# Kernel tuning notes

Measured on AMD Instinct MI355X. Metric: run time of the kernel, lower is better.

The kernel has to match this reference:

```python
import jax, jax.numpy as jnp
import numpy as np

N_NODES = 50000
D = 128
N_POS = 400000
N_NEG = 200000  # N_NODES * neg_k(4)
E = N_POS + N_NEG


def setup_inputs() -> dict:
    key = jax.random.key(0)
    k_x, k_w1, k_w2, k_p = jax.random.split(key, 4)
    x = jax.random.normal(k_x, (N_NODES, D), dtype=jnp.float32)
    # torch nn.Linear params: y = x @ W.T + b
    W1 = jax.random.normal(k_w1, (D, 2 * D), dtype=jnp.float32) * (1.0 / np.sqrt(2 * D))
    b1 = jnp.zeros((D,), dtype=jnp.float32)
    W2 = jax.random.normal(k_w2, (1, D), dtype=jnp.float32) * (1.0 / np.sqrt(D))
    b2 = jnp.zeros((1,), dtype=jnp.float32)
    pairs = jax.random.randint(k_p, (2, E), 0, N_NODES, dtype=jnp.int64)
    labels = jnp.concatenate([jnp.ones((N_POS,), jnp.float32), jnp.zeros((N_NEG,), jnp.float32)])
    return {"x": x, "W1": W1, "b1": b1, "W2": W2, "b2": b2, "labels": labels, "pairs": pairs}


def reference(x, W1, b1, W2, b2, labels, pairs):
    us, vs = pairs[0], pairs[1]
    # edge gather + concat: [E, 2D]
    feats = jnp.concatenate([x[us], x[vs]], axis=-1)
    h = jax.nn.relu(feats @ W1.T + b1)            # [E, D]
    z = (h @ W2.T + b2).ravel()                   # [E] logits
    # binary_cross_entropy_with_logits, mean reduction (numerically stable)
    loss = -jnp.mean(labels * jax.nn.log_sigmoid(z) + (1.0 - labels) * jax.nn.log_sigmoid(-z))
    return loss
```

## Files before the change

### kernel.cpp

```cpp
#include <hip/hip_runtime.h>
#include <hip/hip_fp16.h>

#define D 128
#define TWO_D 256

typedef _Float16 half2v __attribute__((ext_vector_type(2)));
typedef _Float16 half8v __attribute__((ext_vector_type(8)));
typedef float floatx4 __attribute__((ext_vector_type(4)));

__device__ inline unsigned int pkrtz(float a, float b) {
    return __builtin_bit_cast(unsigned int, __builtin_amdgcn_cvt_pkrtz(a, b));
}

__global__ __launch_bounds__(256) void gemm_nodes(
        const float* __restrict__ x, const float* __restrict__ W1,
        const float* __restrict__ b1,
        unsigned char* __restrict__ AB, float* __restrict__ out0, int nNodes) {
    const int tid  = threadIdx.x;
    const int wave = tid >> 6, lane = tid & 63;
    const int quad = lane >> 4, l16 = lane & 15;
    const int nb0  = blockIdx.x * 64;

    if (blockIdx.x == 0 && tid == 0) *out0 = 0.f;

    half8v Bf[4][4];
    float bias[4];
#pragma unroll
    for (int t = 0; t < 4; ++t) {
        const int o = wave * 64 + t * 16 + l16;
        bias[t] = (o < D) ? b1[o] : 0.f;
        const float* wrow = (o < D) ? (W1 + (size_t)o * TWO_D)
                                    : (W1 + (size_t)(o - D) * TWO_D + D);
#pragma unroll
        for (int ks = 0; ks < 4; ++ks) {
            const float* wp = wrow + ks * 32 + quad * 8;
            floatx4 w0 = *(const floatx4*)wp;
            floatx4 w1v = *(const floatx4*)(wp + 4);
            uint4 pk;
            pk.x = pkrtz(w0[0], w0[1]);  pk.y = pkrtz(w0[2], w0[3]);
            pk.z = pkrtz(w1v[0], w1v[1]); pk.w = pkrtz(w1v[2], w1v[3]);
            Bf[t][ks] = __builtin_bit_cast(half8v, pk);
        }
    }

    __shared__ __align__(16) unsigned short xs[16][136];
    __shared__ __align__(16) float ct[16][260];

    const int srow = tid >> 4;
    const int sc8  = tid & 15;

    floatx4 v0, v1;
    {
        const int node = nb0 + srow;
        const int nc = node < nNodes ? node : nNodes - 1;
        const float* xp = x + (size_t)nc * D + sc8 * 8;
        v0 = *(const floatx4*)xp;
        v1 = *(const floatx4*)(xp + 4);
    }

    for (int sub = 0; sub < 4; ++sub) {
        __syncthreads();
        uint4 pk;
        pk.x = pkrtz(v0[0], v0[1]);  pk.y = pkrtz(v0[2], v0[3]);
        pk.z = pkrtz(v1[0], v1[1]);  pk.w = pkrtz(v1[2], v1[3]);
        *(uint4*)&xs[srow][sc8 * 8] = pk;
        __syncthreads();

        if (sub < 3) {
            const int node = nb0 + (sub + 1) * 16 + srow;
            const int nc = node < nNodes ? node : nNodes - 1;
            const float* xp = x + (size_t)nc * D + sc8 * 8;
            v0 = *(const floatx4*)xp;
            v1 = *(const floatx4*)(xp + 4);
        }

        half8v Af[4];
#pragma unroll
        for (int ks = 0; ks < 4; ++ks)
            Af[ks] = *(const half8v*)&xs[l16][ks * 32 + quad * 8];

        floatx4 acc[4];
#pragma unroll
        for (int t = 0; t < 4; ++t) acc[t] = (floatx4){0.f, 0.f, 0.f, 0.f};
#pragma unroll
        for (int ks = 0; ks < 4; ++ks)
#pragma unroll
            for (int t = 0; t < 4; ++t)
                acc[t] = __builtin_amdgcn_mfma_f32_16x16x32_f16(Af[ks], Bf[t][ks], acc[t], 0, 0, 0);

#pragma unroll
        for (int t = 0; t < 4; ++t) {
            const int o = wave * 64 + t * 16 + l16;
#pragma unroll
            for (int r = 0; r < 4; ++r)
                ct[quad * 4 + r][o] = acc[t][r] + bias[t];
        }
        __syncthreads();

        const int nrow = nb0 + sub * 16 + srow;
        if (nrow < nNodes) {
            floatx4 f0 = *(const floatx4*)&ct[srow][sc8 * 16];
            floatx4 f1 = *(const floatx4*)&ct[srow][sc8 * 16 + 4];
            floatx4 f2 = *(const floatx4*)&ct[srow][sc8 * 16 + 8];
            floatx4 f3 = *(const floatx4*)&ct[srow][sc8 * 16 + 12];
            uint4 o8;
            int d;
            d = __builtin_amdgcn_cvt_pk_fp8_f32(f0[0], f0[1], 0, false);
            d = __builtin_amdgcn_cvt_pk_fp8_f32(f0[2], f0[3], d, true);
            o8.x = (unsigned int)d;
            d = __builtin_amdgcn_cvt_pk_fp8_f32(f1[0], f1[1], 0, false);
            d = __builtin_amdgcn_cvt_pk_fp8_f32(f1[2], f1[3], d, true);
            o8.y = (unsigned int)d;
            d = __builtin_amdgcn_cvt_pk_fp8_f32(f2[0], f2[1], 0, false);
            d = __builtin_amdgcn_cvt_pk_fp8_f32(f2[2], f2[3], d, true);
            o8.z = (unsigned int)d;
            d = __builtin_amdgcn_cvt_pk_fp8_f32(f3[0], f3[1], 0, false);
            d = __builtin_amdgcn_cvt_pk_fp8_f32(f3[2], f3[3], d, true);
            o8.w = (unsigned int)d;
            *(uint4*)(AB + (size_t)nrow * TWO_D + sc8 * 16) = o8;
        }
    }
}

__device__ inline float dot4_fp8(unsigned int wa, unsigned int wb,
                                 unsigned int w2lo, unsigned int w2hi, float z) {
#if __has_builtin(__builtin_amdgcn_cvt_pk_f16_fp8)
    half2v a01 = __builtin_bit_cast(half2v, __builtin_amdgcn_cvt_pk_f16_fp8((short)(wa & 0xffffu)));
    half2v a23 = __builtin_bit_cast(half2v, __builtin_amdgcn_cvt_pk_f16_fp8((short)(wa >> 16)));
    half2v b01 = __builtin_bit_cast(half2v, __builtin_amdgcn_cvt_pk_f16_fp8((short)(wb & 0xffffu)));
    half2v b23 = __builtin_bit_cast(half2v, __builtin_amdgcn_cvt_pk_f16_fp8((short)(wb >> 16)));
    half2v zero = {(_Float16)0, (_Float16)0};
    half2v s01 = __builtin_elementwise_max(a01 + b01, zero);
    half2v s23 = __builtin_elementwise_max(a23 + b23, zero);
    z = __builtin_amdgcn_fdot2(s01, __builtin_bit_cast(half2v, w2lo), z, false);
    z = __builtin_amdgcn_fdot2(s23, __builtin_bit_cast(half2v, w2hi), z, false);
#else
    auto a01 = __builtin_amdgcn_cvt_pk_f32_fp8(wa, false);
    auto a23 = __builtin_amdgcn_cvt_pk_f32_fp8(wa, true);
    auto b01 = __builtin_amdgcn_cvt_pk_f32_fp8(wb, false);
    auto b23 = __builtin_amdgcn_cvt_pk_f32_fp8(wb, true);
    half2v wlo = __builtin_bit_cast(half2v, w2lo);
    half2v whi = __builtin_bit_cast(half2v, w2hi);
    float s0 = fmaxf(a01[0] + b01[0], 0.f), s1 = fmaxf(a01[1] + b01[1], 0.f);
    float s2 = fmaxf(a23[0] + b23[0], 0.f), s3 = fmaxf(a23[1] + b23[1], 0.f);
    z = fmaf(s0, (float)wlo[0], z); z = fmaf(s1, (float)wlo[1], z);
    z = fmaf(s2, (float)whi[0], z); z = fmaf(s3, (float)whi[1], z);
#endif
    return z;
}

__device__ inline float edge_dot(const unsigned char* __restrict__ AB,
                                 int u, int v, int l8,
                                 const uint4& w2a, const uint4& w2b) {
    const unsigned char* au = AB + (size_t)u * TWO_D;
    const unsigned char* bv = AB + (size_t)v * TWO_D + D;
    uint4 a4 = *(const uint4*)(au + l8 * 16);
    uint4 b4 = *(const uint4*)(bv + l8 * 16);
    float z = 0.f;
    z = dot4_fp8(a4.x, b4.x, w2a.x, w2a.y, z);
    z = dot4_fp8(a4.y, b4.y, w2a.z, w2a.w, z);
    z = dot4_fp8(a4.z, b4.z, w2b.x, w2b.y, z);
    z = dot4_fp8(a4.w, b4.w, w2b.z, w2b.w, z);
    return z;
}

__device__ inline float red8(float z) {
    z += __shfl_xor(z, 4, 8);
    z += __shfl_xor(z, 2, 8);
    z += __shfl_xor(z, 1, 8);
    return z;
}

__device__ inline float bce(float z, float y) {
    const float t = __expf(-fabsf(z));
    return fmaxf(z, 0.f) - z * y + __logf(1.f + t);
}

__global__ __launch_bounds__(256) void edge_loss(
        const unsigned char* __restrict__ AB,
        const int* __restrict__ pairs,
        const float* __restrict__ labels,
        const float* __restrict__ W2,
        const float* __restrict__ b2,
        float* __restrict__ out, int E, float invE) {
    __shared__ unsigned int w2p[64];
    const int tid = threadIdx.x;
    if (tid < 64) {
        float2 w = *(const float2*)(W2 + tid * 2);
        half2v p = { (_Float16)w.x, (_Float16)w.y };
        w2p[tid] = __builtin_bit_cast(unsigned int, p);
    }
    __syncthreads();
    const int l8 = tid & 7;
    const uint4 w2a = *(const uint4*)&w2p[l8 * 8];
    const uint4 w2b = *(const uint4*)&w2p[l8 * 8 + 4];
    const float bb2 = b2[0];

    float acc = 0.f;
    const int group  = (blockIdx.x * 256 + tid) >> 3;
    const int stride = (gridDim.x * 256) >> 3;

    int e0 = group;
    for (; e0 + stride < E; e0 += 2 * stride) {
        const int e1 = e0 + stride;
        const int u0 = pairs[e0], v0 = pairs[E + e0];
        const int u1 = pairs[e1], v1 = pairs[E + e1];
        float z0 = edge_dot(AB, u0, v0, l8, w2a, w2b);
        float z1 = edge_dot(AB, u1, v1, l8, w2a, w2b);
        z0 = red8(z0) + bb2;
        z1 = red8(z1) + bb2;
        if (l8 == 0) {
            acc += bce(z0, labels[e0]);
            acc += bce(z1, labels[e1]);
        }
    }
    if (e0 < E) {
        const int u0 = pairs[e0], v0 = pairs[E + e0];
        float z0 = edge_dot(AB, u0, v0, l8, w2a, w2b);
        z0 = red8(z0) + bb2;
        if (l8 == 0) acc += bce(z0, labels[e0]);
    }

#pragma unroll
    for (int m = 32; m >= 1; m >>= 1) acc += __shfl_xor(acc, m, 64);
    __shared__ float red[4];
    if ((tid & 63) == 0) red[tid >> 6] = acc;
    __syncthreads();
    if (tid == 0)
        atomicAdd(out, (red[0] + red[1] + red[2] + red[3]) * invE);
}

extern "C" void kernel_launch(void* const* d_in, const int* in_sizes, int n_in,
                              void* d_out, int out_size, void* d_ws, size_t ws_size,
                              hipStream_t stream) {
    const float* x      = (const float*)d_in[0];
    const float* W1     = (const float*)d_in[1];
    const float* b1     = (const float*)d_in[2];
    const float* W2     = (const float*)d_in[3];
    const float* b2     = (const float*)d_in[4];
    const float* labels = (const float*)d_in[5];
    const int*   pairs  = (const int*)d_in[6];

    const int nNodes = in_sizes[0] / D;
    const int E      = in_sizes[5];

    unsigned char* AB = (unsigned char*)d_ws;

    gemm_nodes<<<(nNodes + 63) / 64, 256, 0, stream>>>(x, W1, b1, AB,
                                                        (float*)d_out, nNodes);
    edge_loss<<<2048, 256, 0, stream>>>(AB, pairs, labels, W2, b2,
                                        (float*)d_out, E, 1.0f / (float)E);
}
```

Measured before the change: 137.6 us.

## Batch eight edges per lane group with shuffled indices and prefetched gathers

The edge loss kernel drops the grid-stride loop that handled two edges per iteration. Each 8-lane group now owns eight consecutive edges. The group loads the indices and labels coalesced, one per lane, and broadcasts them with wave shuffles. It issues gathers for four edges ahead of the computation, which raises the number of memory requests in flight. The grid is sized to cover the edges exactly and launch bounds ask for higher occupancy; there is no bounds check for an edge count that is not a multiple of eight.

```diff
diff --git a/kernel.cpp b/kernel.cpp
--- a/kernel.cpp
+++ b/kernel.cpp
@@ -149,13 +149,8 @@
     return z;
 }
 
-__device__ inline float edge_dot(const unsigned char* __restrict__ AB,
-                                 int u, int v, int l8,
-                                 const uint4& w2a, const uint4& w2b) {
-    const unsigned char* au = AB + (size_t)u * TWO_D;
-    const unsigned char* bv = AB + (size_t)v * TWO_D + D;
-    uint4 a4 = *(const uint4*)(au + l8 * 16);
-    uint4 b4 = *(const uint4*)(bv + l8 * 16);
+__device__ inline float dot16(const uint4& a4, const uint4& b4,
+                              const uint4& w2a, const uint4& w2b) {
     float z = 0.f;
     z = dot4_fp8(a4.x, b4.x, w2a.x, w2a.y, z);
     z = dot4_fp8(a4.y, b4.y, w2a.z, w2a.w, z);
@@ -176,7 +171,7 @@
     return fmaxf(z, 0.f) - z * y + __logf(1.f + t);
 }
 
-__global__ __launch_bounds__(256) void edge_loss(
+__global__ __launch_bounds__(256, 8) void edge_loss(
         const unsigned char* __restrict__ AB,
         const int* __restrict__ pairs,
         const float* __restrict__ labels,
@@ -191,34 +186,46 @@
         w2p[tid] = __builtin_bit_cast(unsigned int, p);
     }
     __syncthreads();
-    const int l8 = tid & 7;
+    const int l8   = tid & 7;
+    const int base = tid & 56;
     const uint4 w2a = *(const uint4*)&w2p[l8 * 8];
     const uint4 w2b = *(const uint4*)&w2p[l8 * 8 + 4];
     const float bb2 = b2[0];
 
     float acc = 0.f;
-    const int group  = (blockIdx.x * 256 + tid) >> 3;
-    const int stride = (gridDim.x * 256) >> 3;
-
-    int e0 = group;
-    for (; e0 + stride < E; e0 += 2 * stride) {
-        const int e1 = e0 + stride;
-        const int u0 = pairs[e0], v0 = pairs[E + e0];
-        const int u1 = pairs[e1], v1 = pairs[E + e1];
-        float z0 = edge_dot(AB, u0, v0, l8, w2a, w2b);
-        float z1 = edge_dot(AB, u1, v1, l8, w2a, w2b);
-        z0 = red8(z0) + bb2;
-        z1 = red8(z1) + bb2;
-        if (l8 == 0) {
-            acc += bce(z0, labels[e0]);
-            acc += bce(z1, labels[e1]);
-        }
-    }
+    const int group = (blockIdx.x * 256 + tid) >> 3;
+    const int e0 = group * 8;
     if (e0 < E) {
-        const int u0 = pairs[e0], v0 = pairs[E + e0];
-        float z0 = edge_dot(AB, u0, v0, l8, w2a, w2b);
-        z0 = red8(z0) + bb2;
-        if (l8 == 0) acc += bce(z0, labels[e0]);
+        const int el = e0 + l8;
+        const int u   = pairs[el];
+        const int v   = pairs[E + el];
+        const float lab = labels[el];
+
+        uint4 A[4], B[4];
+#pragma unroll
+        for (int k = 0; k < 4; ++k) {
+            const int uk = __shfl(u, base + k, 64);
+            const int vk = __shfl(v, base + k, 64);
+            A[k] = *(const uint4*)(AB + (size_t)uk * TWO_D + l8 * 16);
+            B[k] = *(const uint4*)(AB + (size_t)vk * TWO_D + D + l8 * 16);
+        }
+#pragma unroll
+        for (int k = 0; k < 4; ++k) {
+            const int uk = __shfl(u, base + 4 + k, 64);
+            const int vk = __shfl(v, base + 4 + k, 64);
+            uint4 A2 = *(const uint4*)(AB + (size_t)uk * TWO_D + l8 * 16);
+            uint4 B2 = *(const uint4*)(AB + (size_t)vk * TWO_D + D + l8 * 16);
+            float z = red8(dot16(A[k], B[k], w2a, w2b)) + bb2;
+            const float labk = __shfl(lab, base + k, 64);
+            if (l8 == 0) acc += bce(z, labk);
+            A[k] = A2; B[k] = B2;
+        }
+#pragma unroll
+        for (int k = 0; k < 4; ++k) {
+            float z = red8(dot16(A[k], B[k], w2a, w2b)) + bb2;
+            const float labk = __shfl(lab, base + 4 + k, 64);
+            if (l8 == 0) acc += bce(z, labk);
+        }
     }
 
 #pragma unroll
@@ -248,6 +255,8 @@
 
     gemm_nodes<<<(nNodes + 63) / 64, 256, 0, stream>>>(x, W1, b1, AB,
                                                         (float*)d_out, nNodes);
-    edge_loss<<<2048, 256, 0, stream>>>(AB, pairs, labels, W2, b2,
-                                        (float*)d_out, E, 1.0f / (float)E);
-}
+    const int nGroups = (E + 7) / 8;
+    const int nBlocks = (nGroups + 31) / 32;
+    edge_loss<<<nBlocks, 256, 0, stream>>>(AB, pairs, labels, W2, b2,
+                                           (float*)d_out, E, 1.0f / (float)E);
+}
```

Result: slower. 168.7 us (+22.6%).
